# Kernel optimization log

Measured on AMD Instinct MI355X. Metric: run time of the kernel, lower is better.

The kernel has to match this reference:

```python
import jax, jax.numpy as jnp
import numpy as np

# Neighbor indices for each of the 24 SMPL joints into the 19 COCO joints,
# derived from coco_nebors + coco_joints_name in the original module.
NEB1 = jnp.array([17, 11, 12, 17, 13, 14, 17, 15, 16, 18, 15, 16, 18, 18, 18, 18, 5, 6, 7, 8, 9, 10, 9, 10])
NEB2 = jnp.array([18, 17, 17, 18, 11, 12, 18, 13, 14, 17, 13, 14, 0, 5, 6, 0, 18, 18, 5, 6, 7, 8, 7, 8])

B, J, SJ, D, H = 8192, 19, 24, 2048, 512  # batch, coco joints, smpl joints, feat dim, lift dim


def setup_inputs() -> dict:
    key = jax.random.key(0)
    ks = jax.random.split(key, 16)
    s = 0.02
    g = 0.01
    f32 = jnp.float32
    return dict(
        joints=jax.random.normal(ks[0], (B, J, 3), f32),
        W_enc=jax.random.normal(ks[1], (J * 3, D), f32) * s,
        b_enc=jnp.zeros((D,), f32),
        W_shape=jax.random.normal(ks[2], (D, 10), f32) * s,
        b_shape=jnp.zeros((10,), f32),
        W_cam=jax.random.normal(ks[3], (D, 3), f32) * s,
        b_cam=jnp.zeros((3,), f32),
        W_phi=jax.random.normal(ks[4], (D, 46), f32) * s,
        b_phi=jnp.zeros((46,), f32),
        W_leaf=jax.random.normal(ks[5], (D, 20), f32) * s,
        b_leaf=jnp.zeros((20,), f32),
        init_shape=jax.random.normal(ks[6], (1, 10), f32) * s,
        init_cam=jax.random.normal(ks[7], (1, 3), f32) * s,
        L1_w=jax.random.normal(ks[8], (SJ, 3, H), f32) * s,   # stacked joint_lifts_1
        L1_b=jnp.zeros((SJ, H), f32),
        L2_w=jax.random.normal(ks[9], (SJ, 3, H), f32) * s,   # stacked joint_lifts_2
        L2_b=jnp.zeros((SJ, H), f32),
        Rf=jax.random.normal(ks[10], (SJ, D, 3), f32) * s * g,
        R1=jax.random.normal(ks[11], (SJ, H, 3), f32) * s * g,
        R2=jax.random.normal(ks[12], (SJ, H, 3), f32) * s * g,
        reg_b=jnp.zeros((SJ, 3), f32),
    )


def reference(joints, W_enc, b_enc, W_shape, b_shape, W_cam, b_cam, W_phi, b_phi,
              W_leaf, b_leaf, init_shape, init_cam, L1_w, L1_b, L2_w, L2_b,
              Rf, R1, R2, reg_b):
    Bc = joints.shape[0]
    joint_feat = joints.reshape(Bc, -1) @ W_enc + b_enc            # [B, 2048]
    pred_shape = joint_feat @ W_shape + b_shape + init_shape       # [B, 10]
    pred_camera = joint_feat @ W_cam + b_cam + init_cam            # [B, 3]
    pred_phi = (joint_feat @ W_phi + b_phi).reshape(Bc, 23, 2)
    pred_leaf = (joint_feat @ W_leaf + b_leaf).reshape(Bc, 5, 4)

    # Batched per-joint neighbor gather + lift (replaces the 24-iteration python loop)
    n1 = joints[:, NEB1]                                           # [B, 24, 3]
    n2 = joints[:, NEB2]                                           # [B, 24, 3]
    l1 = jnp.einsum('bjc,jch->bjh', n1, L1_w) + L1_b               # [B, 24, 512]
    l2 = jnp.einsum('bjc,jch->bjh', n2, L2_w) + L2_b               # [B, 24, 512]

    # reg(concat(joint_feat, l1, l2)) with the 3072-wide weight split into three slices
    pose = (jnp.einsum('bf,jfo->bjo', joint_feat, Rf)
            + jnp.einsum('bjh,jho->bjo', l1, R1)
            + jnp.einsum('bjh,jho->bjo', l2, R2)
            + reg_b)                                               # [B, 24, 3]
    pred_pose = pose - pose[:, :1]                                 # root-center (root_idx_24 = 0)
    return (pred_pose, pred_camera, pred_phi, pred_leaf, pred_shape)
```

## Files before the change

kernel.cpp:

```cpp
#include <hip/hip_runtime.h>

#define NCOL 152
#define NROW 58
#define KC   16
#define KLEN 128
#define NCOLL_BLK (KC * 15)

#define POSE_OFF  0
#define CAM_OFF   589824
#define PHI_OFF   614400
#define LEAF_OFF  991232
#define SHAPE_OFF 1155072

__constant__ int c_NEB1[24] = {17,11,12,17,13,14,17,15,16,18,15,16,18,18,18,18,5,6,7,8,9,10,9,10};
__constant__ int c_NEB2[24] = {18,17,17,18,11,12,18,13,14,17,13,14,0,5,6,0,18,18,5,6,7,8,7,8};

__global__ __launch_bounds__(256) void k_stage1(
    const float* __restrict__ W_enc, const float* __restrict__ b_enc,
    const float* __restrict__ W_shape, const float* __restrict__ W_cam,
    const float* __restrict__ W_phi, const float* __restrict__ W_leaf,
    const float* __restrict__ Rf,
    const float* __restrict__ L1_w, const float* __restrict__ L1_b,
    const float* __restrict__ L2_w, const float* __restrict__ L2_b,
    const float* __restrict__ R1, const float* __restrict__ R2,
    float* __restrict__ partial, float* __restrict__ mfold) {
  __shared__ float sred[4 * 12];
  int bid = blockIdx.x;

  if (bid < NCOLL_BLK) {
    int c = threadIdx.x;
    if (c >= NCOL) return;
    int kc = bid & (KC - 1);
    int rg = bid >> 4;

    const float* base; int stride; bool valid = true;
    if (c < 10)       { base = W_shape + c;      stride = 10; }
    else if (c < 13)  { base = W_cam  + (c-10);  stride = 3;  }
    else if (c < 59)  { base = W_phi  + (c-13);  stride = 46; }
    else if (c < 79)  { base = W_leaf + (c-59);  stride = 20; }
    else if (c < 151) { int p = c-79; base = Rf + (p/3)*6144 + (p%3); stride = 3; }
    else              { base = W_shape; stride = 0; valid = false; }

    int r0 = rg * 4;
    const float* a0 = (r0+0 < 57) ? (W_enc + (r0+0)*2048) : b_enc;
    const float* a1 = (r0+1 < 57) ? (W_enc + (r0+1)*2048) : b_enc;
    const float* a2 = (r0+2 < 57) ? (W_enc + (r0+2)*2048) : b_enc;
    const float* a3 = (r0+3 < 57) ? (W_enc + (r0+3)*2048) : b_enc;

    float acc0=0.f, acc1=0.f, acc2=0.f, acc3=0.f;
    int k0 = kc * KLEN;
    #pragma unroll 8
    for (int k = k0; k < k0 + KLEN; ++k) {
      float v = base[(size_t)k * (size_t)stride];
      acc0 += a0[k]*v; acc1 += a1[k]*v; acc2 += a2[k]*v; acc3 += a3[k]*v;
    }
    if (!valid) { acc0 = acc1 = acc2 = acc3 = 0.f; }

    if (r0+0 < NROW) partial[((r0+0)*KC + kc)*NCOL + c] = acc0;
    if (r0+1 < NROW) partial[((r0+1)*KC + kc)*NCOL + c] = acc1;
    if (r0+2 < NROW) partial[((r0+2)*KC + kc)*NCOL + c] = acc2;
    if (r0+3 < NROW) partial[((r0+3)*KC + kc)*NCOL + c] = acc3;
    return;
  }

  int jm = bid - NCOLL_BLK;
  int j = jm >> 1, m = jm & 1;
  const float* Lw = (m == 0) ? L1_w : L2_w;
  const float* Lb = (m == 0) ? L1_b : L2_b;
  const float* Rm = (m == 0) ? R1   : R2;

  int t = threadIdx.x;
  float acc[12];
  #pragma unroll
  for (int q = 0; q < 12; ++q) acc[q] = 0.f;

  #pragma unroll
  for (int hh = 0; hh < 2; ++hh) {
    int h = t + hh * 256;
    float l0 = Lw[j*1536 + 0*512 + h];
    float l1 = Lw[j*1536 + 1*512 + h];
    float l2 = Lw[j*1536 + 2*512 + h];
    float lb = Lb[j*512 + h];
    float r0 = Rm[j*1536 + h*3 + 0];
    float r1 = Rm[j*1536 + h*3 + 1];
    float r2 = Rm[j*1536 + h*3 + 2];
    acc[0] += l0*r0; acc[1] += l0*r1; acc[2]  += l0*r2;
    acc[3] += l1*r0; acc[4] += l1*r1; acc[5]  += l1*r2;
    acc[6] += l2*r0; acc[7] += l2*r1; acc[8]  += l2*r2;
    acc[9] += lb*r0; acc[10]+= lb*r1; acc[11] += lb*r2;
  }

  #pragma unroll
  for (int q = 0; q < 12; ++q) {
    float v = acc[q];
    v += __shfl_down(v, 32);
    v += __shfl_down(v, 16);
    v += __shfl_down(v, 8);
    v += __shfl_down(v, 4);
    v += __shfl_down(v, 2);
    v += __shfl_down(v, 1);
    acc[q] = v;
  }
  int wv = t >> 6, ln = t & 63;
  if (ln == 0) {
    #pragma unroll
    for (int q = 0; q < 12; ++q) sred[wv*12 + q] = acc[q];
  }
  __syncthreads();
  if (t < 12)
    mfold[jm*12 + t] = sred[0*12 + t] + sred[1*12 + t] + sred[2*12 + t] + sred[3*12 + t];
}

__global__ __launch_bounds__(192) void k_finalize(
    const float* __restrict__ partial, const float* __restrict__ mfold,
    const float* __restrict__ b_shape, const float* __restrict__ b_cam,
    const float* __restrict__ b_phi, const float* __restrict__ b_leaf,
    const float* __restrict__ init_shape, const float* __restrict__ init_cam,
    const float* __restrict__ reg_b, float* __restrict__ Cfull) {
  __shared__ float sbase[NCOL];
  int r = blockIdx.x;
  int t = threadIdx.x;

  if (t < NCOL) {
    float s = 0.f;
    #pragma unroll
    for (int kc = 0; kc < KC; ++kc) s += partial[(r*KC + kc)*NCOL + t];

    if (r == 57) {
      int c = t;
      if (c < 10)       s += b_shape[c] + init_shape[c];
      else if (c < 13)  s += b_cam[c-10] + init_cam[c-10];
      else if (c < 59)  s += b_phi[c-13];
      else if (c < 79)  s += b_leaf[c-59];
      else if (c < 151) s += reg_b[c-79];
    }

    if (t >= 79 && t < 151) {
      int p = t - 79, j = p / 3, o = p % 3;
      if (r < 57) {
        int jr = r / 3, d = r % 3;
        if (c_NEB1[j] == jr) s += mfold[(2*j+0)*12 + d*3 + o];
        if (c_NEB2[j] == jr) s += mfold[(2*j+1)*12 + d*3 + o];
      } else {
        s += mfold[(2*j+0)*12 + 9 + o] + mfold[(2*j+1)*12 + 9 + o];
      }
    }
    sbase[t] = s;
  }
  __syncthreads();

  float v0 = sbase[79], v1 = sbase[80], v2 = sbase[81];
  if (t < NCOL) {
    float s = sbase[t];
    if (t >= 79 && t < 151) {
      int o = (t - 79) % 3;
      s -= (o == 0) ? v0 : ((o == 1) ? v1 : v2);
    }
    Cfull[r*NCOL + t] = s;
  }
}

__device__ __forceinline__ void store_col(float* __restrict__ out, int b, int c, float v) {
  if (c < 10)       out[SHAPE_OFF + b*10 + c]      = v;
  else if (c < 13)  out[CAM_OFF   + b*3  + (c-10)] = v;
  else if (c < 59)  out[PHI_OFF   + b*46 + (c-13)] = v;
  else if (c < 79)  out[LEAF_OFF  + b*20 + (c-59)] = v;
  else              out[POSE_OFF  + b*72 + (c-79)] = v;
}

__global__ __launch_bounds__(256) void k_main(
    const float* __restrict__ joints, const float* __restrict__ Cfull,
    float* __restrict__ out) {
  __shared__ float C[NROW * NCOL];
  for (int i = threadIdx.x; i < (NROW*NCOL)/4; i += 256)
    ((float4*)C)[i] = ((const float4*)Cfull)[i];
  __syncthreads();

  int w = __builtin_amdgcn_readfirstlane((int)(threadIdx.x >> 6));
  int l = (int)(threadIdx.x & 63);
  int b0 = blockIdx.x * 16 + w * 4;

  const float* x0 = joints + (size_t)b0 * 57;
  const float* x1 = x0 + 57;
  const float* x2 = x1 + 57;
  const float* x3 = x2 + 57;

  int lc = (l < 12) ? (2*l) : 22;

  float acc[4][4] = {};
  #pragma unroll
  for (int r = 0; r < 58; ++r) {
    float2 p0 = *(const float2*)&C[r*NCOL + 2*l];
    float2 p1 = *(const float2*)&C[r*NCOL + 128 + lc];
    float xr;
    xr = (r < 57) ? x0[r] : 1.f;
    acc[0][0] += xr*p0.x; acc[0][1] += xr*p0.y; acc[0][2] += xr*p1.x; acc[0][3] += xr*p1.y;
    xr = (r < 57) ? x1[r] : 1.f;
    acc[1][0] += xr*p0.x; acc[1][1] += xr*p0.y; acc[1][2] += xr*p1.x; acc[1][3] += xr*p1.y;
    xr = (r < 57) ? x2[r] : 1.f;
    acc[2][0] += xr*p0.x; acc[2][1] += xr*p0.y; acc[2][2] += xr*p1.x; acc[2][3] += xr*p1.y;
    xr = (r < 57) ? x3[r] : 1.f;
    acc[3][0] += xr*p0.x; acc[3][1] += xr*p0.y; acc[3][2] += xr*p1.x; acc[3][3] += xr*p1.y;
  }

  #pragma unroll
  for (int i = 0; i < 4; ++i) {
    int b = b0 + i;
    store_col(out, b, 2*l,     acc[i][0]);
    store_col(out, b, 2*l + 1, acc[i][1]);
    if (l < 12) {
      store_col(out, b, 128 + 2*l, acc[i][2]);
      if (l < 11) store_col(out, b, 129 + 2*l, acc[i][3]);
    }
  }
}

extern "C" void kernel_launch(void* const* d_in, const int* in_sizes, int n_in,
                              void* d_out, int out_size, void* d_ws, size_t ws_size,
                              hipStream_t stream) {
  const float* joints     = (const float*)d_in[0];
  const float* W_enc      = (const float*)d_in[1];
  const float* b_enc      = (const float*)d_in[2];
  const float* W_shape    = (const float*)d_in[3];
  const float* b_shape    = (const float*)d_in[4];
  const float* W_cam      = (const float*)d_in[5];
  const float* b_cam      = (const float*)d_in[6];
  const float* W_phi      = (const float*)d_in[7];
  const float* b_phi      = (const float*)d_in[8];
  const float* W_leaf     = (const float*)d_in[9];
  const float* b_leaf     = (const float*)d_in[10];
  const float* init_shape = (const float*)d_in[11];
  const float* init_cam   = (const float*)d_in[12];
  const float* L1_w       = (const float*)d_in[13];
  const float* L1_b       = (const float*)d_in[14];
  const float* L2_w       = (const float*)d_in[15];
  const float* L2_b       = (const float*)d_in[16];
  const float* Rf         = (const float*)d_in[17];
  const float* R1         = (const float*)d_in[18];
  const float* R2         = (const float*)d_in[19];
  const float* reg_b      = (const float*)d_in[20];

  float* partial = (float*)d_ws;
  float* Cfull   = partial + NROW*KC*NCOL;
  float* mfold   = Cfull + NROW*NCOL;
  float* outp    = (float*)d_out;

  hipLaunchKernelGGL(k_stage1, dim3(NCOLL_BLK + 48), dim3(256), 0, stream,
                     W_enc, b_enc, W_shape, W_cam, W_phi, W_leaf, Rf,
                     L1_w, L1_b, L2_w, L2_b, R1, R2, partial, mfold);
  hipLaunchKernelGGL(k_finalize, dim3(NROW), dim3(192), 0, stream,
                     partial, mfold, b_shape, b_cam, b_phi, b_leaf,
                     init_shape, init_cam, reg_b, Cfull);
  hipLaunchKernelGGL(k_main, dim3(512), dim3(256), 0, stream,
                     joints, Cfull, outp);
}
```

Baseline: 120.1 us.

## Stage outputs in shared memory for coalesced writes and regroup stage1 rows by five

The main kernel now writes its per-thread results into a shared-memory tile, then writes each output tensor with contiguous, coalesced stores. Before, each thread scattered strided stores through a branchy helper. The bias row is folded into the accumulator initialisation, which removes the 58th loop iteration and its conditional loads. Stage1 now processes five W_enc rows per block instead of four, so fewer blocks are launched, at the cost of more shared memory and an extra barrier in k_main.

```diff
diff --git a/kernel.cpp b/kernel.cpp
--- a/kernel.cpp
+++ b/kernel.cpp
@@ -4,7 +4,8 @@
 #define NROW 58
 #define KC   16
 #define KLEN 128
-#define NCOLL_BLK (KC * 15)
+#define RG   12
+#define NCOLL_BLK (KC * RG)
 
 #define POSE_OFF  0
 #define CAM_OFF   589824
@@ -41,25 +42,27 @@
     else if (c < 151) { int p = c-79; base = Rf + (p/3)*6144 + (p%3); stride = 3; }
     else              { base = W_shape; stride = 0; valid = false; }
 
-    int r0 = rg * 4;
-    const float* a0 = (r0+0 < 57) ? (W_enc + (r0+0)*2048) : b_enc;
-    const float* a1 = (r0+1 < 57) ? (W_enc + (r0+1)*2048) : b_enc;
-    const float* a2 = (r0+2 < 57) ? (W_enc + (r0+2)*2048) : b_enc;
-    const float* a3 = (r0+3 < 57) ? (W_enc + (r0+3)*2048) : b_enc;
-
-    float acc0=0.f, acc1=0.f, acc2=0.f, acc3=0.f;
+    int r0 = rg * 5;
+    const float* a0 = (r0+0 < 57) ? (W_enc + (size_t)(r0+0)*2048) : b_enc;
+    const float* a1 = (r0+1 < 57) ? (W_enc + (size_t)(r0+1)*2048) : b_enc;
+    const float* a2 = (r0+2 < 57) ? (W_enc + (size_t)(r0+2)*2048) : b_enc;
+    const float* a3 = (r0+3 < 57) ? (W_enc + (size_t)(r0+3)*2048) : b_enc;
+    const float* a4 = (r0+4 < 57) ? (W_enc + (size_t)(r0+4)*2048) : b_enc;
+
+    float acc0=0.f, acc1=0.f, acc2=0.f, acc3=0.f, acc4=0.f;
     int k0 = kc * KLEN;
     #pragma unroll 8
     for (int k = k0; k < k0 + KLEN; ++k) {
       float v = base[(size_t)k * (size_t)stride];
-      acc0 += a0[k]*v; acc1 += a1[k]*v; acc2 += a2[k]*v; acc3 += a3[k]*v;
-    }
-    if (!valid) { acc0 = acc1 = acc2 = acc3 = 0.f; }
+      acc0 += a0[k]*v; acc1 += a1[k]*v; acc2 += a2[k]*v; acc3 += a3[k]*v; acc4 += a4[k]*v;
+    }
+    if (!valid) { acc0 = acc1 = acc2 = acc3 = acc4 = 0.f; }
 
     if (r0+0 < NROW) partial[((r0+0)*KC + kc)*NCOL + c] = acc0;
     if (r0+1 < NROW) partial[((r0+1)*KC + kc)*NCOL + c] = acc1;
     if (r0+2 < NROW) partial[((r0+2)*KC + kc)*NCOL + c] = acc2;
     if (r0+3 < NROW) partial[((r0+3)*KC + kc)*NCOL + c] = acc3;
+    if (r0+4 < NROW) partial[((r0+4)*KC + kc)*NCOL + c] = acc4;
     return;
   }
 
@@ -160,59 +163,72 @@
   }
 }
 
-__device__ __forceinline__ void store_col(float* __restrict__ out, int b, int c, float v) {
-  if (c < 10)       out[SHAPE_OFF + b*10 + c]      = v;
-  else if (c < 13)  out[CAM_OFF   + b*3  + (c-10)] = v;
-  else if (c < 59)  out[PHI_OFF   + b*46 + (c-13)] = v;
-  else if (c < 79)  out[LEAF_OFF  + b*20 + (c-59)] = v;
-  else              out[POSE_OFF  + b*72 + (c-79)] = v;
-}
-
 __global__ __launch_bounds__(256) void k_main(
     const float* __restrict__ joints, const float* __restrict__ Cfull,
     float* __restrict__ out) {
   __shared__ float C[NROW * NCOL];
+  __shared__ float T[16 * NCOL];
   for (int i = threadIdx.x; i < (NROW*NCOL)/4; i += 256)
     ((float4*)C)[i] = ((const float4*)Cfull)[i];
   __syncthreads();
 
   int w = __builtin_amdgcn_readfirstlane((int)(threadIdx.x >> 6));
   int l = (int)(threadIdx.x & 63);
-  int b0 = blockIdx.x * 16 + w * 4;
-
-  const float* x0 = joints + (size_t)b0 * 57;
+  int b0 = blockIdx.x * 16;
+  int row0 = w * 4;
+
+  const float* x0 = joints + (size_t)(b0 + row0) * 57;
   const float* x1 = x0 + 57;
   const float* x2 = x1 + 57;
   const float* x3 = x2 + 57;
 
   int lc = (l < 12) ? (2*l) : 22;
 
-  float acc[4][4] = {};
-  #pragma unroll
-  for (int r = 0; r < 58; ++r) {
+  float2 q0 = *(const float2*)&C[57*NCOL + 2*l];
+  float2 q1 = *(const float2*)&C[57*NCOL + 128 + lc];
+  float acc[4][4];
+  #pragma unroll
+  for (int i = 0; i < 4; ++i) {
+    acc[i][0] = q0.x; acc[i][1] = q0.y; acc[i][2] = q1.x; acc[i][3] = q1.y;
+  }
+
+  #pragma unroll
+  for (int r = 0; r < 57; ++r) {
     float2 p0 = *(const float2*)&C[r*NCOL + 2*l];
     float2 p1 = *(const float2*)&C[r*NCOL + 128 + lc];
     float xr;
-    xr = (r < 57) ? x0[r] : 1.f;
+    xr = x0[r];
     acc[0][0] += xr*p0.x; acc[0][1] += xr*p0.y; acc[0][2] += xr*p1.x; acc[0][3] += xr*p1.y;
-    xr = (r < 57) ? x1[r] : 1.f;
+    xr = x1[r];
     acc[1][0] += xr*p0.x; acc[1][1] += xr*p0.y; acc[1][2] += xr*p1.x; acc[1][3] += xr*p1.y;
-    xr = (r < 57) ? x2[r] : 1.f;
+    xr = x2[r];
     acc[2][0] += xr*p0.x; acc[2][1] += xr*p0.y; acc[2][2] += xr*p1.x; acc[2][3] += xr*p1.y;
-    xr = (r < 57) ? x3[r] : 1.f;
+    xr = x3[r];
     acc[3][0] += xr*p0.x; acc[3][1] += xr*p0.y; acc[3][2] += xr*p1.x; acc[3][3] += xr*p1.y;
   }
 
   #pragma unroll
   for (int i = 0; i < 4; ++i) {
-    int b = b0 + i;
-    store_col(out, b, 2*l,     acc[i][0]);
-    store_col(out, b, 2*l + 1, acc[i][1]);
+    int tr = row0 + i;
+    *(float2*)&T[tr*NCOL + 2*l] = make_float2(acc[i][0], acc[i][1]);
     if (l < 12) {
-      store_col(out, b, 128 + 2*l, acc[i][2]);
-      if (l < 11) store_col(out, b, 129 + 2*l, acc[i][3]);
-    }
-  }
+      T[tr*NCOL + 128 + 2*l] = acc[i][2];
+      if (l < 11) T[tr*NCOL + 129 + 2*l] = acc[i][3];
+    }
+  }
+  __syncthreads();
+
+#define WRITEOUT(OFF, COLS, CBASE)                                        \
+  for (int idx = threadIdx.x; idx < 16*(COLS); idx += 256) {              \
+    out[(OFF) + (size_t)b0*(COLS) + idx] =                                \
+        T[(idx/(COLS))*NCOL + (CBASE) + (idx % (COLS))];                  \
+  }
+  WRITEOUT(POSE_OFF,  72, 79)
+  WRITEOUT(CAM_OFF,    3, 10)
+  WRITEOUT(PHI_OFF,   46, 13)
+  WRITEOUT(LEAF_OFF,  20, 59)
+  WRITEOUT(SHAPE_OFF, 10,  0)
+#undef WRITEOUT
 }
 
 extern "C" void kernel_launch(void* const* d_in, const int* in_sizes, int n_in,
```

Measured after the change: 122.8 us. 1.02x slower.
